# Optimization experiments

Measured on AMD Instinct MI355X. Metric: run time of the kernel, lower is better.

Reference implementation:

```python
import jax, jax.numpy as jnp
import numpy as np


def setup_inputs() -> dict:
    key = jax.random.key(0)
    ks = jax.random.split(key, 5)
    B, H, W, C = 4, 64, 64, 256
    Ck = C // 8  # key/query channels = 32
    x = jax.random.normal(ks[0], (B, H, W, C), dtype=jnp.float32)
    # 1x1 conv kernels (spec_norm=False -> plain conv), Glorot-ish scaling
    Wf = jax.random.normal(ks[1], (C, Ck), dtype=jnp.float32) * (1.0 / np.sqrt(C))
    Wg = jax.random.normal(ks[2], (C, Ck), dtype=jnp.float32) * (1.0 / np.sqrt(C))
    Wh = jax.random.normal(ks[3], (C, C), dtype=jnp.float32) * (1.0 / np.sqrt(C))
    bf = jnp.zeros((Ck,), dtype=jnp.float32)
    bg = jnp.zeros((Ck,), dtype=jnp.float32)
    bh = jnp.zeros((C,), dtype=jnp.float32)
    # gamma is zero-init in the module; use a nonzero value so the attention
    # branch actually contributes to the output (as after some training).
    gamma = jnp.float32(0.5)
    return {"x": x, "Wf": Wf, "bf": bf, "Wg": Wg, "bg": bg,
            "Wh": Wh, "bh": bh, "gamma": gamma}


def reference(x, Wf, bf, Wg, bg, Wh, bh, gamma):
    B, H, W, C = x.shape
    N = H * W
    xf = x.reshape(B, N, C)  # hw_flatten of input (1x1 conv == per-pixel matmul)
    f = xf @ Wf + bf         # [B, N, Ck] keys
    g = xf @ Wg + bg         # [B, N, Ck] queries
    h = xf @ Wh + bh         # [B, N, C]  values
    s = jnp.einsum('bqk,bnk->bqn', g, f)  # [B, N, N] scores (g @ f^T)
    b = jax.nn.softmax(s, axis=-1)
    o = jnp.einsum('bqn,bnc->bqc', b, h)  # [B, N, C]
    # in-channels == nfilters, so scale(x) = x (identity)
    y = gamma * o.reshape(B, H, W, C) + x
    return y
```

## Files before the change

### kernel.cpp

```cpp
#include <hip/hip_runtime.h>
#include <stdint.h>

#define B_ 4
#define N_ 4096
#define C_ 256
#define LOG2E 1.44269504088896340736f
#define SOFT_OFF 88.0f

typedef float f32x4 __attribute__((ext_vector_type(4)));
typedef float f32x16 __attribute__((ext_vector_type(16)));
typedef short s16x8 __attribute__((ext_vector_type(8)));
typedef __bf16 bf16x8 __attribute__((ext_vector_type(8)));
typedef _Float16 f16x8 __attribute__((ext_vector_type(8)));

static __device__ __forceinline__ unsigned short f2bf(float f) {
    union { float f; uint32_t u; } v; v.f = f;
    return (unsigned short)((v.u + 0x7FFFu + ((v.u >> 16) & 1u)) >> 16);
}
static __device__ __forceinline__ unsigned short f2bf_rh(float f) {
    union { float f; uint32_t u; } v; v.f = f;
    return (unsigned short)((v.u + 0x8000u) >> 16);
}

__global__ __launch_bounds__(256) void wprep(
    const float* __restrict__ Wf, const float* __restrict__ Wg,
    const float* __restrict__ Wh, _Float16* __restrict__ WT)
{
    __shared__ float tile[64][33];
    const int t = blockIdx.x, kc = blockIdx.y, tid = threadIdx.x;
    const float* src; int stride;
    if (t == 0)      { src = Wf;                stride = 32;  }
    else if (t == 1) { src = Wg;                stride = 32;  }
    else             { src = Wh + (t - 2) * 32; stride = 256; }

    const int c = tid & 31, a = tid >> 5;
    #pragma unroll
    for (int p = 0; p < 8; p++) {
        int kk = p * 8 + a;
        tile[kk][c] = src[(size_t)(kc * 64 + kk) * stride + c];
    }
    __syncthreads();
    const int kk = tid & 63, aa = tid >> 6;
    #pragma unroll
    for (int p = 0; p < 8; p++) {
        int cc = p * 4 + aa;
        WT[(size_t)(t * 32 + cc) * 256 + kc * 64 + kk] = (_Float16)tile[kk][cc];
    }
}

__global__ __launch_bounds__(256, 3) void proj_kernel(
    const float* __restrict__ x,
    const float* __restrict__ bfp, const float* __restrict__ bgp,
    const float* __restrict__ bhp,
    const _Float16* __restrict__ WT,
    _Float16* __restrict__ qf16, _Float16* __restrict__ kf16,
    unsigned short* __restrict__ v_t)
{
    __shared__ __align__(16) unsigned short pool[16384 + 6144];
    _Float16* xs = (_Float16*)pool;
    _Float16* wts[2] = { (_Float16*)(pool + 16384),
                         (_Float16*)(pool + 16384 + 3072) };
    unsigned short* tbuf = pool + 16384;

    const int tid  = threadIdx.x;
    const int lane = tid & 63;
    const int wave = tid >> 6;
    const int m_   = lane & 31;
    const int k8   = lane >> 5;
    const int row0 = blockIdx.x * 64;
    const int half = blockIdx.y;
    const int b    = row0 >> 12;
    const int n0   = row0 & 4095;
    const int npair = half ? 128 : 192;

    #pragma unroll
    for (int i = 0; i < 8; i++) {
        int r  = 8 * i + (tid >> 5);
        int c5 = tid & 31;
        const f32x4* src = (const f32x4*)(x + (size_t)(row0 + r) * 256 + c5 * 8);
        f32x4 a = src[0], c4 = src[1];
        f16x8 h = { (_Float16)a.x, (_Float16)a.y, (_Float16)a.z, (_Float16)a.w,
                    (_Float16)c4.x, (_Float16)c4.y, (_Float16)c4.z, (_Float16)c4.w };
        int chunk = (((r >> 5) * 16 + (c5 >> 1)) * 2 + (c5 & 1)) * 32
                  + ((r & 31) ^ (c5 & 7));
        *(f16x8*)(xs + chunk * 8) = h;
    }
    if (tid < npair) {
        const _Float16* s = WT + (size_t)(half * 192 + tid) * 256;
        f16x8 w0 = *(const f16x8*)(s), w1 = *(const f16x8*)(s + 8);
        *(f16x8*)(wts[0] + (0 * 192 + tid) * 8) = w0;
        *(f16x8*)(wts[0] + (1 * 192 + tid) * 8) = w1;
    }
    __syncthreads();

    const int rowsub = wave & 1;
    const int tg     = wave >> 1;
    const int ntile  = (half == 0) ? 3 : 2;
    const int lt0    = (half == 0) ? tg * 3 : tg * 2;
    const int t_base = (half == 0) ? tg * 3 : 6 + tg * 2;

    f32x16 acc[3];
    #pragma unroll
    for (int t = 0; t < 3; t++)
        #pragma unroll
        for (int i = 0; i < 16; i++) acc[t][i] = 0.f;

    for (int ks = 0; ks < 16; ks++) {
        const int cur = ks & 1, nxt = cur ^ 1;
        const int ksn = (ks < 15) ? ks + 1 : 15;
        f16x8 w0, w1;
        if (tid < npair) {
            const _Float16* s = WT + (size_t)(half * 192 + tid) * 256 + ksn * 16;
            w0 = *(const f16x8*)(s); w1 = *(const f16x8*)(s + 8);
        }
        f16x8 A = *(const f16x8*)(xs + ((((rowsub * 16 + ks) * 2 + k8) * 32)
                                        + (m_ ^ ((ks * 2 + k8) & 7))) * 8);
        #pragma unroll
        for (int t = 0; t < 3; t++) {
            if (t >= ntile) break;
            f16x8 Bv = *(const f16x8*)(wts[cur] + (k8 * 192 + (lt0 + t) * 32 + m_) * 8);
            acc[t] = __builtin_amdgcn_mfma_f32_32x32x16_f16(A, Bv, acc[t], 0, 0, 0);
        }
        __syncthreads();
        if (tid < npair) {
            *(f16x8*)(wts[nxt] + (0 * 192 + tid) * 8) = w0;
            *(f16x8*)(wts[nxt] + (1 * 192 + tid) * 8) = w1;
        }
        __syncthreads();
    }

    #pragma unroll
    for (int t = 0; t < 3; t++) {
        if (t >= ntile) break;
        int tile = t_base + t;
        if (tile < 2) {
            float bias = (tile == 0) ? bfp[m_] : bgp[m_];
            _Float16* dst = (tile == 0) ? kf16 : qf16;
            #pragma unroll
            for (int r = 0; r < 16; r++) {
                int m = (r & 3) + 8 * (r >> 2) + 4 * k8;
                int row = row0 + rowsub * 32 + m;
                dst[(size_t)row * 32 + m_] = (_Float16)(acc[t][r] + bias);
            }
        } else {
            int ch = (tile - 2) * 32 + m_;
            float bias = bhp[ch];
            unsigned short* buf = tbuf + wave * (32 * 40);
            #pragma unroll
            for (int u = 0; u < 8; u++) {
                int r = 2 * u;
                int m = (r & 3) + 8 * (r >> 2) + 4 * k8;
                uint32_t v = (uint32_t)f2bf(acc[t][r] + bias)
                           | ((uint32_t)f2bf(acc[t][r + 1] + bias) << 16);
                *(uint32_t*)(buf + m_ * 40 + m) = v;
            }
            #pragma unroll
            for (int u = 0; u < 2; u++) {
                int idx2 = u * 64 + lane;
                int chr = idx2 >> 2, q8 = idx2 & 3;
                s16x8 vv = *(const s16x8*)(buf + chr * 40 + q8 * 8);
                int colh = (tile - 2) * 32 + chr;
                *(s16x8*)(v_t + ((size_t)(b * 256 + colh)) * 4096
                               + n0 + rowsub * 32 + q8 * 8) = vv;
            }
        }
    }
}

__global__ __launch_bounds__(512, 4) void attn_kernel(
    const _Float16* __restrict__ qf16, const _Float16* __restrict__ kf16,
    const unsigned short* __restrict__ v_t,
    const float* __restrict__ x, const float* __restrict__ gamma_p,
    float* __restrict__ out)
{
    __shared__ __align__(16) unsigned short hT_s[2][8192];
    __shared__ __align__(16) unsigned short P_s[2][2048];
    __shared__ float l_s[2][2][32];

    const int tid  = threadIdx.x;
    const int lane = tid & 63;
    const int wave = tid >> 6;
    const int qsub = wave & 1;
    const int chsl = wave >> 1;
    const int m_   = lane & 31;
    const int k8   = lane >> 5;
    const int qt   = blockIdx.x;
    const int chg  = blockIdx.y;
    const int b    = blockIdx.z;
    const size_t bn = (size_t)b * N_;
    const int ch0  = chg * 128;
    const bool is_s = (wave < 4);
    const int ksub  = wave >> 1;

    const int hi0 = tid >> 3;
    const int hko = tid & 7;
    const size_t hrow0 = ((size_t)(b * 256 + ch0 + hi0)) * 4096 + hko * 8;
    const size_t hrow1 = ((size_t)(b * 256 + ch0 + 64 + hi0)) * 4096 + hko * 8;
    const int hc0 = (hko * 128 + (hi0 ^ hko)) * 8;
    const int hc1 = (hko * 128 + ((64 + hi0) ^ hko)) * 8;

    f16x8 Aq0, Aq1, Kc0, Kc1;
    if (is_s) {
        const int qrow = qt * 64 + qsub * 32 + m_;
        Aq0 = *(const f16x8*)(qf16 + (bn + qrow) * 32 + k8 * 8);
        Aq1 = *(const f16x8*)(qf16 + (bn + qrow) * 32 + 16 + k8 * 8);
        const _Float16* kp = kf16 + (bn + ksub * 32 + m_) * 32;
        Kc0 = *(const f16x8*)(kp + k8 * 8);
        Kc1 = *(const f16x8*)(kp + 16 + k8 * 8);
    }

    {
        s16x8 h0 = *(const s16x8*)(v_t + hrow0);
        s16x8 h1 = *(const s16x8*)(v_t + hrow1);
        *(s16x8*)(&hT_s[0][hc0]) = h0;
        *(s16x8*)(&hT_s[0][hc1]) = h1;
    }
    __syncthreads();

    f32x16 acc;
    float l_acc[16];
    #pragma unroll
    for (int i = 0; i < 16; i++) { acc[i] = 0.f; l_acc[i] = 0.f; }

    for (int kt = 0; kt < N_ / 64; kt++) {
        const int cur = kt & 1, nxt = cur ^ 1;
        const int ktn = (kt < 63) ? kt + 1 : 63;
        s16x8 h0 = *(const s16x8*)(v_t + (size_t)ktn * 64 + hrow0);
        s16x8 h1 = *(const s16x8*)(v_t + (size_t)ktn * 64 + hrow1);
        f16x8 Kn0, Kn1;
        if (is_s) {
            const _Float16* kp = kf16 + (bn + ktn * 64 + ksub * 32 + m_) * 32;
            Kn0 = *(const f16x8*)(kp + k8 * 8);
            Kn1 = *(const f16x8*)(kp + 16 + k8 * 8);
        }
        if (is_s) {
            f32x16 s;
            #pragma unroll
            for (int i = 0; i < 16; i++) s[i] = 0.f;
            s = __builtin_amdgcn_mfma_f32_32x32x16_f16(Aq0, Kc0, s, 0, 0, 0);
            s = __builtin_amdgcn_mfma_f32_32x32x16_f16(Aq1, Kc1, s, 0, 0, 0);
            unsigned short* Pb = P_s[qsub];
            const int octet = ksub * 4 + (m_ >> 3);
            const int kofs = m_ & 7;
            #pragma unroll
            for (int r = 0; r < 16; r++) {
                float p = __builtin_amdgcn_exp2f(fmaf(s[r], LOG2E, -SOFT_OFF));
                l_acc[r] += p;
                int m = (r & 3) + 8 * (r >> 2) + 4 * k8;
                Pb[(octet * 32 + (m ^ (octet & 3))) * 8 + kofs] = f2bf_rh(p);
            }
        }
        __syncthreads();

        const unsigned short* Pr = P_s[qsub];
        const unsigned short* Hc = hT_s[cur];
        #pragma unroll
        for (int kstep = 0; kstep < 4; kstep++) {
            int oct = kstep * 2 + k8;
            bf16x8 Ap = *(const bf16x8*)(Pr + (oct * 32 + (m_ ^ (oct & 3))) * 8);
            bf16x8 Bv = *(const bf16x8*)(Hc + (oct * 128 + ((chsl * 32 + m_) ^ oct)) * 8);
            acc = __builtin_amdgcn_mfma_f32_32x32x16_bf16(Ap, Bv, acc, 0, 0, 0);
        }
        *(s16x8*)(&hT_s[nxt][hc0]) = h0;
        *(s16x8*)(&hT_s[nxt][hc1]) = h1;
        if (is_s) { Kc0 = Kn0; Kc1 = Kn1; }
        __syncthreads();
    }

    if (is_s) {
        #pragma unroll
        for (int off = 1; off < 32; off <<= 1)
            #pragma unroll
            for (int r = 0; r < 16; r++)
                l_acc[r] += __shfl_xor(l_acc[r], off, 64);
        if (m_ == 0) {
            #pragma unroll
            for (int r = 0; r < 16; r++) {
                int q = (r & 3) + 8 * (r >> 2) + 4 * k8;
                l_s[qsub][ksub][q] = l_acc[r];
            }
        }
    }
    __syncthreads();

    const float gamma = *gamma_p;
    #pragma unroll
    for (int r = 0; r < 16; r++) {
        int q = (r & 3) + 8 * (r >> 2) + 4 * k8;
        float l = l_s[qsub][0][q] + l_s[qsub][1][q];
        size_t idx = (bn + qt * 64 + qsub * 32 + q) * 256 + ch0 + chsl * 32 + m_;
        out[idx] = gamma * (acc[r] / l) + x[idx];
    }
}

extern "C" void kernel_launch(void* const* d_in, const int* in_sizes, int n_in,
                              void* d_out, int out_size, void* d_ws, size_t ws_size,
                              hipStream_t stream) {
    const float* x   = (const float*)d_in[0];
    const float* Wf  = (const float*)d_in[1];
    const float* bfp = (const float*)d_in[2];
    const float* Wg  = (const float*)d_in[3];
    const float* bgp = (const float*)d_in[4];
    const float* Wh  = (const float*)d_in[5];
    const float* bhp = (const float*)d_in[6];
    const float* gam = (const float*)d_in[7];
    float* out = (float*)d_out;

    unsigned char* ws = (unsigned char*)d_ws;
    const size_t MB = 1 << 20;
    _Float16* WT    = (_Float16*)(ws);
    _Float16* qf16  = (_Float16*)(ws + 1 * MB);
    _Float16* kf16  = (_Float16*)(ws + 2 * MB);
    unsigned short* v_t = (unsigned short*)(ws + 3 * MB);

    wprep<<<dim3(10, 4), dim3(256), 0, stream>>>(Wf, Wg, Wh, WT);
    proj_kernel<<<dim3(256, 2), dim3(256), 0, stream>>>(
        x, bfp, bgp, bhp, WT, qf16, kf16, v_t);
    attn_kernel<<<dim3(64, 2, 4), dim3(512), 0, stream>>>(
        qf16, kf16, v_t, x, gam, out);
}
```

Measured before the change: 164.9 us.

## Store V in MFMA fragment order and load it directly into registers

The projection kernel now writes the value tensor in a pre-swizzled fragment layout, so the attention kernel can load each MFMA B operand straight from global memory into registers. This removes the double-buffered LDS staging of V and the LDS reads in the attention loop. The projection kernel is also restructured: each wave takes one 32-column tile, weights are read directly from global into registers, and the grid grows to 5 column groups so its LDS weight double-buffering and per-step barriers go away. The trade-off is that attention now issues more global/L2 loads per wave, because V fragments are shared across the two query-sub waves rather than read once into shared memory.

```diff
diff --git a/kernel.cpp b/kernel.cpp
--- a/kernel.cpp
+++ b/kernel.cpp
@@ -54,13 +54,10 @@
     const float* __restrict__ bhp,
     const _Float16* __restrict__ WT,
     _Float16* __restrict__ qf16, _Float16* __restrict__ kf16,
-    unsigned short* __restrict__ v_t)
+    unsigned short* __restrict__ v_frag)
 {
-    __shared__ __align__(16) unsigned short pool[16384 + 6144];
-    _Float16* xs = (_Float16*)pool;
-    _Float16* wts[2] = { (_Float16*)(pool + 16384),
-                         (_Float16*)(pool + 16384 + 3072) };
-    unsigned short* tbuf = pool + 16384;
+    __shared__ __align__(16) _Float16 xs[64 * 256];
+    __shared__ __align__(16) unsigned short tbuf[4][32 * 40];
 
     const int tid  = threadIdx.x;
     const int lane = tid & 63;
@@ -68,10 +65,9 @@
     const int m_   = lane & 31;
     const int k8   = lane >> 5;
     const int row0 = blockIdx.x * 64;
-    const int half = blockIdx.y;
     const int b    = row0 >> 12;
     const int n0   = row0 & 4095;
-    const int npair = half ? 128 : 192;
+    const int kt   = n0 >> 6;
 
     #pragma unroll
     for (int i = 0; i < 8; i++) {
@@ -81,99 +77,79 @@
         f32x4 a = src[0], c4 = src[1];
         f16x8 h = { (_Float16)a.x, (_Float16)a.y, (_Float16)a.z, (_Float16)a.w,
                     (_Float16)c4.x, (_Float16)c4.y, (_Float16)c4.z, (_Float16)c4.w };
-        int chunk = (((r >> 5) * 16 + (c5 >> 1)) * 2 + (c5 & 1)) * 32
-                  + ((r & 31) ^ (c5 & 7));
+        int chunk = (((r >> 5) * 32 + c5)) * 32 + ((r & 31) ^ (c5 & 7));
         *(f16x8*)(xs + chunk * 8) = h;
     }
-    if (tid < npair) {
-        const _Float16* s = WT + (size_t)(half * 192 + tid) * 256;
-        f16x8 w0 = *(const f16x8*)(s), w1 = *(const f16x8*)(s + 8);
-        *(f16x8*)(wts[0] + (0 * 192 + tid) * 8) = w0;
-        *(f16x8*)(wts[0] + (1 * 192 + tid) * 8) = w1;
-    }
     __syncthreads();
 
     const int rowsub = wave & 1;
-    const int tg     = wave >> 1;
-    const int ntile  = (half == 0) ? 3 : 2;
-    const int lt0    = (half == 0) ? tg * 3 : tg * 2;
-    const int t_base = (half == 0) ? tg * 3 : 6 + tg * 2;
-
-    f32x16 acc[3];
-    #pragma unroll
-    for (int t = 0; t < 3; t++)
-        #pragma unroll
-        for (int i = 0; i < 16; i++) acc[t][i] = 0.f;
-
-    for (int ks = 0; ks < 16; ks++) {
-        const int cur = ks & 1, nxt = cur ^ 1;
-        const int ksn = (ks < 15) ? ks + 1 : 15;
-        f16x8 w0, w1;
-        if (tid < npair) {
-            const _Float16* s = WT + (size_t)(half * 192 + tid) * 256 + ksn * 16;
-            w0 = *(const f16x8*)(s); w1 = *(const f16x8*)(s + 8);
-        }
-        f16x8 A = *(const f16x8*)(xs + ((((rowsub * 16 + ks) * 2 + k8) * 32)
-                                        + (m_ ^ ((ks * 2 + k8) & 7))) * 8);
-        #pragma unroll
-        for (int t = 0; t < 3; t++) {
-            if (t >= ntile) break;
-            f16x8 Bv = *(const f16x8*)(wts[cur] + (k8 * 192 + (lt0 + t) * 32 + m_) * 8);
-            acc[t] = __builtin_amdgcn_mfma_f32_32x32x16_f16(A, Bv, acc[t], 0, 0, 0);
-        }
-        __syncthreads();
-        if (tid < npair) {
-            *(f16x8*)(wts[nxt] + (0 * 192 + tid) * 8) = w0;
-            *(f16x8*)(wts[nxt] + (1 * 192 + tid) * 8) = w1;
-        }
-        __syncthreads();
-    }
-
-    #pragma unroll
-    for (int t = 0; t < 3; t++) {
-        if (t >= ntile) break;
-        int tile = t_base + t;
-        if (tile < 2) {
-            float bias = (tile == 0) ? bfp[m_] : bgp[m_];
-            _Float16* dst = (tile == 0) ? kf16 : qf16;
-            #pragma unroll
-            for (int r = 0; r < 16; r++) {
-                int m = (r & 3) + 8 * (r >> 2) + 4 * k8;
-                int row = row0 + rowsub * 32 + m;
-                dst[(size_t)row * 32 + m_] = (_Float16)(acc[t][r] + bias);
-            }
-        } else {
-            int ch = (tile - 2) * 32 + m_;
-            float bias = bhp[ch];
-            unsigned short* buf = tbuf + wave * (32 * 40);
-            #pragma unroll
-            for (int u = 0; u < 8; u++) {
-                int r = 2 * u;
-                int m = (r & 3) + 8 * (r >> 2) + 4 * k8;
-                uint32_t v = (uint32_t)f2bf(acc[t][r] + bias)
-                           | ((uint32_t)f2bf(acc[t][r + 1] + bias) << 16);
-                *(uint32_t*)(buf + m_ * 40 + m) = v;
-            }
-            #pragma unroll
-            for (int u = 0; u < 2; u++) {
-                int idx2 = u * 64 + lane;
-                int chr = idx2 >> 2, q8 = idx2 & 3;
-                s16x8 vv = *(const s16x8*)(buf + chr * 40 + q8 * 8);
-                int colh = (tile - 2) * 32 + chr;
-                *(s16x8*)(v_t + ((size_t)(b * 256 + colh)) * 4096
-                               + n0 + rowsub * 32 + q8 * 8) = vv;
-            }
+    const int tile   = blockIdx.y * 2 + (wave >> 1);
+    const _Float16* wb = WT + (size_t)(tile * 32 + m_) * 256 + k8 * 8;
+
+    f32x16 acc;
+    #pragma unroll
+    for (int i = 0; i < 16; i++) acc[i] = 0.f;
+
+    f16x8 Bb[2][4];
+    #pragma unroll
+    for (int j = 0; j < 4; j++) Bb[0][j] = *(const f16x8*)(wb + j * 16);
+    #pragma unroll
+    for (int g4 = 0; g4 < 4; g4++) {
+        const int cur = g4 & 1, nxt = cur ^ 1;
+        if (g4 < 3)
+            #pragma unroll
+            for (int j = 0; j < 4; j++)
+                Bb[nxt][j] = *(const f16x8*)(wb + (g4 * 4 + 4 + j) * 16);
+        #pragma unroll
+        for (int j = 0; j < 4; j++) {
+            int ks = g4 * 4 + j;
+            f16x8 A = *(const f16x8*)(xs + ((rowsub * 32 + ks * 2 + k8) * 32
+                                            + (m_ ^ ((ks * 2 + k8) & 7))) * 8);
+            acc = __builtin_amdgcn_mfma_f32_32x32x16_f16(A, Bb[cur][j], acc, 0, 0, 0);
+        }
+    }
+
+    if (tile < 2) {
+        float bias = (tile == 0) ? bfp[m_] : bgp[m_];
+        _Float16* dst = (tile == 0) ? kf16 : qf16;
+        #pragma unroll
+        for (int r = 0; r < 16; r++) {
+            int m = (r & 3) + 8 * (r >> 2) + 4 * k8;
+            int row = row0 + rowsub * 32 + m;
+            dst[(size_t)row * 32 + m_] = (_Float16)(acc[r] + bias);
+        }
+    } else {
+        const int ht   = tile - 2;
+        const int chgv = ht >> 2, chslv = ht & 3;
+        float bias = bhp[ht * 32 + m_];
+        unsigned short* buf = tbuf[wave];
+        #pragma unroll
+        for (int u = 0; u < 8; u++) {
+            int r = 2 * u;
+            int m = (r & 3) + 8 * (r >> 2) + 4 * k8;
+            uint32_t v = (uint32_t)f2bf(acc[r] + bias)
+                       | ((uint32_t)f2bf(acc[r + 1] + bias) << 16);
+            *(uint32_t*)(buf + m_ * 40 + m) = v;
+        }
+        #pragma unroll
+        for (int u = 0; u < 2; u++) {
+            int idx2 = u * 64 + lane;
+            int chr = idx2 >> 2, q8 = idx2 & 3;
+            s16x8 vv = *(const s16x8*)(buf + chr * 40 + q8 * 8);
+            int oct = rowsub * 4 + q8;
+            size_t e = (((((size_t)(b * 2 + chgv) * 64 + kt) * 8 + oct) * 4
+                          + chslv) * 32 + chr) * 8;
+            *(s16x8*)(v_frag + e) = vv;
         }
     }
 }
 
 __global__ __launch_bounds__(512, 4) void attn_kernel(
     const _Float16* __restrict__ qf16, const _Float16* __restrict__ kf16,
-    const unsigned short* __restrict__ v_t,
+    const unsigned short* __restrict__ v_frag,
     const float* __restrict__ x, const float* __restrict__ gamma_p,
     float* __restrict__ out)
 {
-    __shared__ __align__(16) unsigned short hT_s[2][8192];
     __shared__ __align__(16) unsigned short P_s[2][2048];
     __shared__ float l_s[2][2][32];
 
@@ -192,12 +168,8 @@
     const bool is_s = (wave < 4);
     const int ksub  = wave >> 1;
 
-    const int hi0 = tid >> 3;
-    const int hko = tid & 7;
-    const size_t hrow0 = ((size_t)(b * 256 + ch0 + hi0)) * 4096 + hko * 8;
-    const size_t hrow1 = ((size_t)(b * 256 + ch0 + 64 + hi0)) * 4096 + hko * 8;
-    const int hc0 = (hko * 128 + (hi0 ^ hko)) * 8;
-    const int hc1 = (hko * 128 + ((64 + hi0) ^ hko)) * 8;
+    const unsigned short* vb = v_frag + (size_t)(b * 2 + chg) * 524288
+                             + (size_t)k8 * 1024 + chsl * 256 + m_ * 8;
 
     f16x8 Aq0, Aq1, Kc0, Kc1;
     if (is_s) {
@@ -209,24 +181,17 @@
         Kc1 = *(const f16x8*)(kp + 16 + k8 * 8);
     }
 
-    {
-        s16x8 h0 = *(const s16x8*)(v_t + hrow0);
-        s16x8 h1 = *(const s16x8*)(v_t + hrow1);
-        *(s16x8*)(&hT_s[0][hc0]) = h0;
-        *(s16x8*)(&hT_s[0][hc1]) = h1;
-    }
-    __syncthreads();
-
     f32x16 acc;
     float l_acc[16];
     #pragma unroll
     for (int i = 0; i < 16; i++) { acc[i] = 0.f; l_acc[i] = 0.f; }
 
     for (int kt = 0; kt < N_ / 64; kt++) {
-        const int cur = kt & 1, nxt = cur ^ 1;
         const int ktn = (kt < 63) ? kt + 1 : 63;
-        s16x8 h0 = *(const s16x8*)(v_t + (size_t)ktn * 64 + hrow0);
-        s16x8 h1 = *(const s16x8*)(v_t + (size_t)ktn * 64 + hrow1);
+        bf16x8 Bv[4];
+        #pragma unroll
+        for (int kstep = 0; kstep < 4; kstep++)
+            Bv[kstep] = *(const bf16x8*)(vb + (size_t)kt * 8192 + kstep * 2048);
         f16x8 Kn0, Kn1;
         if (is_s) {
             const _Float16* kp = kf16 + (bn + ktn * 64 + ksub * 32 + m_) * 32;
@@ -253,16 +218,12 @@
         __syncthreads();
 
         const unsigned short* Pr = P_s[qsub];
-        const unsigned short* Hc = hT_s[cur];
         #pragma unroll
         for (int kstep = 0; kstep < 4; kstep++) {
             int oct = kstep * 2 + k8;
             bf16x8 Ap = *(const bf16x8*)(Pr + (oct * 32 + (m_ ^ (oct & 3))) * 8);
-            bf16x8 Bv = *(const bf16x8*)(Hc + (oct * 128 + ((chsl * 32 + m_) ^ oct)) * 8);
-            acc = __builtin_amdgcn_mfma_f32_32x32x16_bf16(Ap, Bv, acc, 0, 0, 0);
-        }
-        *(s16x8*)(&hT_s[nxt][hc0]) = h0;
-        *(s16x8*)(&hT_s[nxt][hc1]) = h1;
+            acc = __builtin_amdgcn_mfma_f32_32x32x16_bf16(Ap, Bv[kstep], acc, 0, 0, 0);
+        }
         if (is_s) { Kc0 = Kn0; Kc1 = Kn1; }
         __syncthreads();
     }
@@ -311,11 +272,11 @@
     _Float16* WT    = (_Float16*)(ws);
     _Float16* qf16  = (_Float16*)(ws + 1 * MB);
     _Float16* kf16  = (_Float16*)(ws + 2 * MB);
-    unsigned short* v_t = (unsigned short*)(ws + 3 * MB);
+    unsigned short* v_frag = (unsigned short*)(ws + 3 * MB);
 
     wprep<<<dim3(10, 4), dim3(256), 0, stream>>>(Wf, Wg, Wh, WT);
-    proj_kernel<<<dim3(256, 2), dim3(256), 0, stream>>>(
-        x, bfp, bgp, bhp, WT, qf16, kf16, v_t);
+    proj_kernel<<<dim3(256, 5), dim3(256), 0, stream>>>(
+        x, bfp, bgp, bhp, WT, qf16, kf16, v_frag);
     attn_kernel<<<dim3(64, 2, 4), dim3(512), 0, stream>>>(
-        qf16, kf16, v_t, x, gam, out);
-}
+        qf16, kf16, v_frag, x, gam, out);
+}
```

After: 158.7 us. -3.8%, faster.
